# Performance work log

Hardware: AMD Instinct MI355X
Metric: run time of the kernel (lower is better)

## Reference

```python
import jax, jax.numpy as jnp
import numpy as np

N, E, D_IN, H = 40000, 640000, 128, 128
R, B = 8, 30  # num_relations = 2*n_speakers**2, num_bases


def setup_inputs() -> dict:
    key = jax.random.key(0)
    ks = jax.random.split(key, 10)
    node_features = jax.random.normal(ks[0], (N, D_IN), jnp.float32)
    edge_index = jax.random.randint(ks[1], (2, E), 0, N)
    edge_type = jax.random.randint(ks[2], (E,), 0, R)
    edge_norm = jax.random.uniform(ks[3], (E,), jnp.float32)
    s_in = 1.0 / np.sqrt(D_IN)
    s_h = 1.0 / np.sqrt(H)
    basis = jax.random.normal(ks[4], (B, D_IN, H), jnp.float32) * s_in
    comp = jax.random.normal(ks[5], (R, B), jnp.float32) * (1.0 / np.sqrt(B))
    root = jax.random.normal(ks[6], (D_IN, H), jnp.float32) * s_in
    bias1 = jnp.zeros((H,), jnp.float32)
    w_rel = jax.random.normal(ks[7], (H, H), jnp.float32) * s_h
    w_root2 = jax.random.normal(ks[8], (H, H), jnp.float32) * s_h
    bias2 = jnp.zeros((H,), jnp.float32)
    return dict(node_features=node_features, edge_index=edge_index,
                edge_norm=edge_norm, edge_type=edge_type,
                basis=basis, comp=comp, root=root, bias1=bias1,
                w_rel=w_rel, w_root2=w_root2, bias2=bias2)


def reference(node_features, edge_index, edge_norm, edge_type,
              basis, comp, root, bias1, w_rel, w_root2, bias2):
    n = node_features.shape[0]
    src, dst = edge_index[0], edge_index[1]  # messages flow src -> dst

    # ---- RGCNConv (basis decomposition, mean aggregation, root + bias) ----
    # Per-relation weights from bases: [R, D_in, H]
    w = jnp.einsum('rb,bio->rio', comp, basis)
    # Transform all nodes by every relation once (avoids per-edge matmul): [R, N, H]
    xw = jnp.einsum('nd,rdo->rno', node_features, w)
    msgs = xw[edge_type, src]                                  # [E, H]
    agg = jax.ops.segment_sum(msgs, dst, num_segments=n)       # [N, H]
    deg = jax.ops.segment_sum(jnp.ones_like(dst, dtype=node_features.dtype),
                              dst, num_segments=n)
    agg = agg / jnp.maximum(deg, 1.0)[:, None]                 # mean aggregation
    h = agg + node_features @ root + bias1                     # [N, H]

    # ---- GraphConv (add aggregation): W_rel * sum_j x_j + W_root * x_i + b ----
    nbr = jax.ops.segment_sum(h[src], dst, num_segments=n)     # [N, H]
    out = nbr @ w_rel + h @ w_root2 + bias2
    return out
```

## Files before the change

### kernel.cpp

```cpp
#include <hip/hip_runtime.h>
#include <stdint.h>

#define DH 128
#define NB 30
#define NR 8

typedef short bf16x8 __attribute__((ext_vector_type(8)));
typedef float f32x4 __attribute__((ext_vector_type(4)));

static __device__ __forceinline__ unsigned short f2bf(float f) {
    unsigned u = __float_as_uint(f);
    u += 0x7fffu + ((u >> 16) & 1u);
    return (unsigned short)(u >> 16);
}

__global__ __launch_bounds__(256) void k_cvtx(const float* __restrict__ x,
                                              unsigned short* __restrict__ xbf, int n4) {
    int i = blockIdx.x * blockDim.x + threadIdx.x;
    if (i < n4) {
        float4 v = ((const float4*)x)[i];
        ushort4 u;
        u.x = f2bf(v.x); u.y = f2bf(v.y); u.z = f2bf(v.z); u.w = f2bf(v.w);
        ((ushort4*)xbf)[i] = u;
    }
}

__global__ __launch_bounds__(128) void k_wprep(const float* __restrict__ comp,
                                               const float* __restrict__ basis,
                                               const float* __restrict__ root,
                                               const float* __restrict__ wrel,
                                               const float* __restrict__ wroot2,
                                               unsigned short* __restrict__ wallT,
                                               unsigned short* __restrict__ WT2) {
    int o = threadIdx.x;
    int i = blockIdx.x;
    int y = blockIdx.y;
    if (y < NR) {
        float s = 0.f;
        #pragma unroll
        for (int b = 0; b < NB; ++b)
            s += comp[y * NB + b] * basis[((size_t)b * DH + i) * DH + o];
        wallT[((size_t)y * DH + o) * DH + i] = f2bf(s);
    } else if (y == NR) {
        wallT[((size_t)NR * DH + o) * DH + i] = f2bf(root[i * DH + o]);
    } else {
        const float* W = (y == NR + 2) ? wroot2 : wrel;
        WT2[((size_t)(y - NR - 1) * DH + o) * DH + i] = f2bf(W[i * DH + o]);
    }
}

__global__ void k_hist(const int* __restrict__ dst, int E, int* __restrict__ deg) {
    int e = blockIdx.x * blockDim.x + threadIdx.x;
    if (e < E) atomicAdd(&deg[dst[e]], 1);
}

__global__ __launch_bounds__(1024) void k_scan1(const int* __restrict__ deg, int n, int total_n,
                                                int* __restrict__ offsets, int* __restrict__ partial) {
    __shared__ int s[1024];
    int tid = threadIdx.x;
    int i = blockIdx.x * 1024 + tid;
    int v = (i < n) ? deg[i] : 0;
    s[tid] = v;
    __syncthreads();
    for (int off = 1; off < 1024; off <<= 1) {
        int t = (tid >= off) ? s[tid - off] : 0;
        __syncthreads();
        s[tid] += t;
        __syncthreads();
    }
    if (i < total_n) offsets[i] = s[tid] - v;
    if (tid == 1023) partial[blockIdx.x] = s[1023];
}

__global__ void k_scan2(int* __restrict__ partial, int nb) {
    if (threadIdx.x == 0) {
        int run = 0;
        for (int b = 0; b < nb; ++b) { int t = partial[b]; partial[b] = run; run += t; }
    }
}

__global__ __launch_bounds__(1024) void k_scan3(int* __restrict__ offsets,
                                                const int* __restrict__ partial, int total_n) {
    int i = blockIdx.x * 1024 + threadIdx.x;
    if (i < total_n) offsets[i] += partial[blockIdx.x];
}

__global__ void k_scatter(const int* __restrict__ src, const int* __restrict__ dstA,
                          const int* __restrict__ etype, int E,
                          const int* __restrict__ offsets, int* __restrict__ cursor,
                          unsigned* __restrict__ sorted) {
    int e = blockIdx.x * blockDim.x + threadIdx.x;
    if (e >= E) return;
    int d = dstA[e];
    int pos = offsets[d] + atomicAdd(&cursor[d], 1);
    sorted[pos] = (unsigned)src[e] | ((unsigned)etype[e] << 17);
}

__global__ __launch_bounds__(256) void k_gemm1m(const unsigned short* __restrict__ Xbf,
                                                const unsigned short* __restrict__ wallT,
                                                const float* __restrict__ bias1,
                                                int Nn,
                                                unsigned short* __restrict__ xw,
                                                unsigned short* __restrict__ hb) {
    __shared__ __align__(16) unsigned short As[128][136];
    __shared__ __align__(16) unsigned short Bs[128][136];
    const int tid = threadIdx.x;
    const int wave = tid >> 6, lane = tid & 63;
    const int r = blockIdx.y;
    const int rowbase = blockIdx.x * 128;
    const unsigned short* WT = wallT + (size_t)r * DH * DH;

    #pragma unroll
    for (int it = 0; it < 8; ++it) {
        int c = it * 256 + tid;
        int row = c >> 4, col = c & 15;
        int rg = rowbase + row; if (rg >= Nn) rg = Nn - 1;
        *(uint4*)&As[row][col * 8] = *(const uint4*)&Xbf[(size_t)rg * DH + col * 8];
        *(uint4*)&Bs[row][col * 8] = *(const uint4*)&WT[(size_t)row * DH + col * 8];
    }
    __syncthreads();

    f32x4 acc[2][8];
    #pragma unroll
    for (int mt = 0; mt < 2; ++mt)
        #pragma unroll
        for (int nt = 0; nt < 8; ++nt) acc[mt][nt] = (f32x4)0.f;

    const int lq = lane >> 4, lr = lane & 15;
    #pragma unroll
    for (int ks = 0; ks < 4; ++ks) {
        const int ko = ks * 32 + lq * 8;
        bf16x8 a0 = *(const bf16x8*)&As[wave * 32 + lr][ko];
        bf16x8 a1 = *(const bf16x8*)&As[wave * 32 + 16 + lr][ko];
        #pragma unroll
        for (int nt = 0; nt < 8; ++nt) {
            bf16x8 b = *(const bf16x8*)&Bs[nt * 16 + lr][ko];
            acc[0][nt] = __builtin_amdgcn_mfma_f32_16x16x32_bf16(a0, b, acc[0][nt], 0, 0, 0);
            acc[1][nt] = __builtin_amdgcn_mfma_f32_16x16x32_bf16(a1, b, acc[1][nt], 0, 0, 0);
        }
    }

    float bv[8];
    #pragma unroll
    for (int nt = 0; nt < 8; ++nt) bv[nt] = (r == NR) ? bias1[nt * 16 + lr] : 0.f;
    #pragma unroll
    for (int mt = 0; mt < 2; ++mt)
        #pragma unroll
        for (int nt = 0; nt < 8; ++nt)
            #pragma unroll
            for (int reg = 0; reg < 4; ++reg) {
                int ml = wave * 32 + mt * 16 + lq * 4 + reg;
                As[ml][nt * 16 + lr] = f2bf(acc[mt][nt][reg] + bv[nt]);
            }
    __syncthreads();
    unsigned short* dst = (r < NR) ? xw + ((size_t)r * Nn + rowbase) * DH
                                   : hb + (size_t)rowbase * DH;
    #pragma unroll
    for (int it = 0; it < 8; ++it) {
        int c = it * 256 + tid;
        int row = c >> 4, col = c & 15;
        if (rowbase + row < Nn)
            *(uint4*)&dst[(size_t)row * DH + col * 8] = *(uint4*)&As[row][col * 8];
    }
}

__global__ __launch_bounds__(256) void k_agg1(const int* __restrict__ offsets,
                                              const unsigned* __restrict__ sorted,
                                              const unsigned* __restrict__ xw32,
                                              const unsigned* __restrict__ hb32,
                                              int Nn, unsigned* __restrict__ hbf) {
    int w = (blockIdx.x * blockDim.x + threadIdx.x) >> 6;
    if (w >= Nn) return;
    int lane = threadIdx.x & 63;
    int s = offsets[w], e = offsets[w + 1];
    float ax = 0.f, ay = 0.f;
    for (int p = s; p < e; p += 16) {
        unsigned pk[16]; float m[16];
        #pragma unroll
        for (int j = 0; j < 16; ++j) {
            int q = p + j; bool v = q < e;
            pk[j] = sorted[v ? q : e - 1];
            m[j] = v ? 1.f : 0.f;
        }
        unsigned u[16];
        #pragma unroll
        for (int j = 0; j < 16; ++j)
            u[j] = xw32[((size_t)(pk[j] >> 17) * Nn + (pk[j] & 0x1FFFFu)) * 64 + lane];
        #pragma unroll
        for (int j = 0; j < 16; ++j) {
            ax = fmaf(m[j], __uint_as_float(u[j] << 16), ax);
            ay = fmaf(m[j], __uint_as_float(u[j] & 0xffff0000u), ay);
        }
    }
    float invd = 1.0f / fmaxf((float)(e - s), 1.0f);
    unsigned hv = hb32[(size_t)w * 64 + lane];
    float hx = __uint_as_float(hv << 16) + ax * invd;
    float hy = __uint_as_float(hv & 0xffff0000u) + ay * invd;
    hbf[(size_t)w * 64 + lane] = (unsigned)f2bf(hx) | ((unsigned)f2bf(hy) << 16);
}

__global__ __launch_bounds__(256) void k_agg2(const int* __restrict__ offsets,
                                              const unsigned* __restrict__ sorted,
                                              const unsigned* __restrict__ hbf32,
                                              int Nn, unsigned* __restrict__ nbrbf) {
    int w = (blockIdx.x * blockDim.x + threadIdx.x) >> 6;
    if (w >= Nn) return;
    int lane = threadIdx.x & 63;
    int s = offsets[w], e = offsets[w + 1];
    float ax = 0.f, ay = 0.f;
    for (int p = s; p < e; p += 16) {
        unsigned pk[16]; float m[16];
        #pragma unroll
        for (int j = 0; j < 16; ++j) {
            int q = p + j; bool v = q < e;
            pk[j] = sorted[v ? q : e - 1];
            m[j] = v ? 1.f : 0.f;
        }
        unsigned u[16];
        #pragma unroll
        for (int j = 0; j < 16; ++j)
            u[j] = hbf32[(size_t)(pk[j] & 0x1FFFFu) * 64 + lane];
        #pragma unroll
        for (int j = 0; j < 16; ++j) {
            ax = fmaf(m[j], __uint_as_float(u[j] << 16), ax);
            ay = fmaf(m[j], __uint_as_float(u[j] & 0xffff0000u), ay);
        }
    }
    nbrbf[(size_t)w * 64 + lane] = (unsigned)f2bf(ax) | ((unsigned)f2bf(ay) << 16);
}

__global__ __launch_bounds__(256) void k_gemm2m(const unsigned short* __restrict__ nbrbf,
                                                const unsigned short* __restrict__ hbf,
                                                const unsigned short* __restrict__ WT2,
                                                const float* __restrict__ bias2,
                                                int Nn, float* __restrict__ out) {
    __shared__ __align__(16) unsigned short As[128][136];
    __shared__ __align__(16) unsigned short Bs[128][136];
    const int tid = threadIdx.x;
    const int wave = tid >> 6, lane = tid & 63;
    const int rowbase = blockIdx.x * 128;
    const int lq = lane >> 4, lr = lane & 15;

    f32x4 acc[2][8];
    #pragma unroll
    for (int mt = 0; mt < 2; ++mt)
        #pragma unroll
        for (int nt = 0; nt < 8; ++nt) acc[mt][nt] = (f32x4)0.f;

    for (int ph = 0; ph < 2; ++ph) {
        const unsigned short* A = ph ? hbf : nbrbf;
        const unsigned short* WT = WT2 + (size_t)ph * DH * DH;
        if (ph) __syncthreads();
        #pragma unroll
        for (int it = 0; it < 8; ++it) {
            int c = it * 256 + tid;
            int row = c >> 4, col = c & 15;
            int rg = rowbase + row; if (rg >= Nn) rg = Nn - 1;
            *(uint4*)&As[row][col * 8] = *(const uint4*)&A[(size_t)rg * DH + col * 8];
            *(uint4*)&Bs[row][col * 8] = *(const uint4*)&WT[(size_t)row * DH + col * 8];
        }
        __syncthreads();
        #pragma unroll
        for (int ks = 0; ks < 4; ++ks) {
            const int ko = ks * 32 + lq * 8;
            bf16x8 a0 = *(const bf16x8*)&As[wave * 32 + lr][ko];
            bf16x8 a1 = *(const bf16x8*)&As[wave * 32 + 16 + lr][ko];
            #pragma unroll
            for (int nt = 0; nt < 8; ++nt) {
                bf16x8 b = *(const bf16x8*)&Bs[nt * 16 + lr][ko];
                acc[0][nt] = __builtin_amdgcn_mfma_f32_16x16x32_bf16(a0, b, acc[0][nt], 0, 0, 0);
                acc[1][nt] = __builtin_amdgcn_mfma_f32_16x16x32_bf16(a1, b, acc[1][nt], 0, 0, 0);
            }
        }
    }

    float bv[8];
    #pragma unroll
    for (int nt = 0; nt < 8; ++nt) bv[nt] = bias2[nt * 16 + lr];
    #pragma unroll
    for (int mt = 0; mt < 2; ++mt)
        #pragma unroll
        for (int nt = 0; nt < 8; ++nt)
            #pragma unroll
            for (int reg = 0; reg < 4; ++reg) {
                int m = rowbase + wave * 32 + mt * 16 + lq * 4 + reg;
                if (m < Nn) out[(size_t)m * DH + nt * 16 + lr] = acc[mt][nt][reg] + bv[nt];
            }
}

extern "C" void kernel_launch(void* const* d_in, const int* in_sizes, int n_in,
                              void* d_out, int out_size, void* d_ws, size_t ws_size,
                              hipStream_t stream) {
    const float* x      = (const float*)d_in[0];
    const int*   eidx   = (const int*)d_in[1];
    const int*   etype  = (const int*)d_in[3];
    const float* basis  = (const float*)d_in[4];
    const float* comp   = (const float*)d_in[5];
    const float* root   = (const float*)d_in[6];
    const float* bias1  = (const float*)d_in[7];
    const float* wrel   = (const float*)d_in[8];
    const float* wroot2 = (const float*)d_in[9];
    const float* bias2  = (const float*)d_in[10];
    float* out = (float*)d_out;

    const int N = in_sizes[0] / DH;
    const int E = in_sizes[3];
    const int* srcA = eidx;
    const int* dstA = eidx + E;

    char* ws = (char*)d_ws;
    size_t off = 0;
    auto alloc = [&](size_t bytes) -> void* {
        void* p = (void*)(ws + off);
        off += (bytes + 255) & ~(size_t)255;
        return p;
    };
    int* deg           = (int*)alloc((size_t)N * 4);
    int* cursor        = (int*)alloc((size_t)N * 4);
    int* offsets       = (int*)alloc((size_t)(N + 1) * 4);
    int* partial       = (int*)alloc(256 * 4);
    unsigned* sorted   = (unsigned*)alloc((size_t)E * 4);
    unsigned short* wallT = (unsigned short*)alloc((size_t)(NR + 1) * DH * DH * 2);
    unsigned short* WT2   = (unsigned short*)alloc((size_t)2 * DH * DH * 2);
    unsigned short* Xbf   = (unsigned short*)alloc((size_t)N * DH * 2);
    unsigned short* xw    = (unsigned short*)alloc((size_t)NR * N * DH * 2);
    unsigned short* hb    = (unsigned short*)alloc((size_t)N * DH * 2);
    unsigned* hbf      = (unsigned*)alloc((size_t)N * (DH / 2) * 4);
    unsigned* nbrbf    = (unsigned*)alloc((size_t)N * (DH / 2) * 4);
    (void)ws_size; (void)n_in; (void)out_size;

    hipMemsetAsync(deg, 0, (size_t)N * 8, stream);

    k_cvtx<<<(N * DH / 4 + 255) / 256, 256, 0, stream>>>(x, Xbf, N * DH / 4);
    k_wprep<<<dim3(DH, NR + 3), DH, 0, stream>>>(comp, basis, root, wrel, wroot2, wallT, WT2);
    k_hist<<<(E + 255) / 256, 256, 0, stream>>>(dstA, E, deg);

    const int totn = N + 1;
    const int nsb = (totn + 1023) / 1024;
    k_scan1<<<nsb, 1024, 0, stream>>>(deg, N, totn, offsets, partial);
    k_scan2<<<1, 64, 0, stream>>>(partial, nsb);
    k_scan3<<<nsb, 1024, 0, stream>>>(offsets, partial, totn);
    k_scatter<<<(E + 255) / 256, 256, 0, stream>>>(srcA, dstA, etype, E, offsets, cursor, sorted);

    const int gx = (N + 127) / 128;
    k_gemm1m<<<dim3(gx, NR + 1), 256, 0, stream>>>(Xbf, wallT, bias1, N, xw, hb);
    k_agg1<<<(N * 64) / 256, 256, 0, stream>>>(offsets, sorted, (const unsigned*)xw,
                                               (const unsigned*)hb, N, hbf);
    k_agg2<<<(N * 64) / 256, 256, 0, stream>>>(offsets, sorted, hbf, N, nbrbf);
    k_gemm2m<<<gx, 256, 0, stream>>>((const unsigned short*)nbrbf, (const unsigned short*)hbf,
                                     WT2, bias2, N, out);
}
```

Baseline: 267.0 us.

## Store per-relation transformed features as FP8 and gather two edges per wave

The first GEMM now writes per-relation transformed node features as packed FP8 instead of bf16, halving the bytes in the largest intermediate buffer and in the random gathers of the first aggregation. Each GEMM block also reuses its loaded X tile across three relation weight matrices (grid y reduced to 3). The aggregation kernel splits each wave into two halves that handle alternating edges with 4 features per lane, then combines them with a cross-half shuffle. FP8 quantization of messages reduces numerical precision and may risk tolerance failures.

```diff
diff --git a/kernel.cpp b/kernel.cpp
--- a/kernel.cpp
+++ b/kernel.cpp
@@ -7,12 +7,15 @@
 
 typedef short bf16x8 __attribute__((ext_vector_type(8)));
 typedef float f32x4 __attribute__((ext_vector_type(4)));
+typedef float f32x2 __attribute__((ext_vector_type(2)));
 
 static __device__ __forceinline__ unsigned short f2bf(float f) {
     unsigned u = __float_as_uint(f);
     u += 0x7fffu + ((u >> 16) & 1u);
     return (unsigned short)(u >> 16);
 }
+static __device__ __forceinline__ float bflo(unsigned u) { return __uint_as_float(u << 16); }
+static __device__ __forceinline__ float bfhi(unsigned u) { return __uint_as_float(u & 0xffff0000u); }
 
 __global__ __launch_bounds__(256) void k_cvtx(const float* __restrict__ x,
                                               unsigned short* __restrict__ xbf, int n4) {
@@ -100,15 +103,15 @@
                                                 const unsigned short* __restrict__ wallT,
                                                 const float* __restrict__ bias1,
                                                 int Nn,
-                                                unsigned short* __restrict__ xw,
+                                                unsigned* __restrict__ xw8,
                                                 unsigned short* __restrict__ hb) {
     __shared__ __align__(16) unsigned short As[128][136];
     __shared__ __align__(16) unsigned short Bs[128][136];
     const int tid = threadIdx.x;
     const int wave = tid >> 6, lane = tid & 63;
-    const int r = blockIdx.y;
+    const int g = blockIdx.y;
     const int rowbase = blockIdx.x * 128;
-    const unsigned short* WT = wallT + (size_t)r * DH * DH;
+    const int lq = lane >> 4, lr = lane & 15;
 
     #pragma unroll
     for (int it = 0; it < 8; ++it) {
@@ -116,87 +119,131 @@
         int row = c >> 4, col = c & 15;
         int rg = rowbase + row; if (rg >= Nn) rg = Nn - 1;
         *(uint4*)&As[row][col * 8] = *(const uint4*)&Xbf[(size_t)rg * DH + col * 8];
-        *(uint4*)&Bs[row][col * 8] = *(const uint4*)&WT[(size_t)row * DH + col * 8];
-    }
-    __syncthreads();
-
-    f32x4 acc[2][8];
-    #pragma unroll
-    for (int mt = 0; mt < 2; ++mt)
-        #pragma unroll
-        for (int nt = 0; nt < 8; ++nt) acc[mt][nt] = (f32x4)0.f;
-
-    const int lq = lane >> 4, lr = lane & 15;
-    #pragma unroll
-    for (int ks = 0; ks < 4; ++ks) {
-        const int ko = ks * 32 + lq * 8;
-        bf16x8 a0 = *(const bf16x8*)&As[wave * 32 + lr][ko];
-        bf16x8 a1 = *(const bf16x8*)&As[wave * 32 + 16 + lr][ko];
-        #pragma unroll
-        for (int nt = 0; nt < 8; ++nt) {
-            bf16x8 b = *(const bf16x8*)&Bs[nt * 16 + lr][ko];
-            acc[0][nt] = __builtin_amdgcn_mfma_f32_16x16x32_bf16(a0, b, acc[0][nt], 0, 0, 0);
-            acc[1][nt] = __builtin_amdgcn_mfma_f32_16x16x32_bf16(a1, b, acc[1][nt], 0, 0, 0);
-        }
-    }
-
-    float bv[8];
-    #pragma unroll
-    for (int nt = 0; nt < 8; ++nt) bv[nt] = (r == NR) ? bias1[nt * 16 + lr] : 0.f;
-    #pragma unroll
-    for (int mt = 0; mt < 2; ++mt)
-        #pragma unroll
-        for (int nt = 0; nt < 8; ++nt)
-            #pragma unroll
-            for (int reg = 0; reg < 4; ++reg) {
-                int ml = wave * 32 + mt * 16 + lq * 4 + reg;
-                As[ml][nt * 16 + lr] = f2bf(acc[mt][nt][reg] + bv[nt]);
-            }
-    __syncthreads();
-    unsigned short* dst = (r < NR) ? xw + ((size_t)r * Nn + rowbase) * DH
-                                   : hb + (size_t)rowbase * DH;
-    #pragma unroll
-    for (int it = 0; it < 8; ++it) {
-        int c = it * 256 + tid;
-        int row = c >> 4, col = c & 15;
-        if (rowbase + row < Nn)
-            *(uint4*)&dst[(size_t)row * DH + col * 8] = *(uint4*)&As[row][col * 8];
+    }
+
+    for (int rr = 0; rr < 3; ++rr) {
+        const int r = g * 3 + rr;
+        const unsigned short* WT = wallT + (size_t)r * DH * DH;
+        if (rr) __syncthreads();
+        #pragma unroll
+        for (int it = 0; it < 8; ++it) {
+            int c = it * 256 + tid;
+            int row = c >> 4, col = c & 15;
+            *(uint4*)&Bs[row][col * 8] = *(const uint4*)&WT[(size_t)row * DH + col * 8];
+        }
+        __syncthreads();
+
+        f32x4 acc[2][8];
+        #pragma unroll
+        for (int mt = 0; mt < 2; ++mt)
+            #pragma unroll
+            for (int nt = 0; nt < 8; ++nt) acc[mt][nt] = (f32x4)0.f;
+
+        #pragma unroll
+        for (int ks = 0; ks < 4; ++ks) {
+            const int ko = ks * 32 + lq * 8;
+            bf16x8 a0 = *(const bf16x8*)&As[wave * 32 + lr][ko];
+            bf16x8 a1 = *(const bf16x8*)&As[wave * 32 + 16 + lr][ko];
+            #pragma unroll
+            for (int nt = 0; nt < 8; ++nt) {
+                bf16x8 b = *(const bf16x8*)&Bs[nt * 16 + lr][ko];
+                acc[0][nt] = __builtin_amdgcn_mfma_f32_16x16x32_bf16(a0, b, acc[0][nt], 0, 0, 0);
+                acc[1][nt] = __builtin_amdgcn_mfma_f32_16x16x32_bf16(a1, b, acc[1][nt], 0, 0, 0);
+            }
+        }
+        __syncthreads();
+
+        float bv[8];
+        #pragma unroll
+        for (int nt = 0; nt < 8; ++nt) bv[nt] = (r == NR) ? bias1[nt * 16 + lr] : 0.f;
+        #pragma unroll
+        for (int mt = 0; mt < 2; ++mt)
+            #pragma unroll
+            for (int nt = 0; nt < 8; ++nt)
+                #pragma unroll
+                for (int reg = 0; reg < 4; ++reg) {
+                    int ml = wave * 32 + mt * 16 + lq * 4 + reg;
+                    Bs[ml][nt * 16 + lr] = f2bf(acc[mt][nt][reg] + bv[nt]);
+                }
+        __syncthreads();
+
+        if (r < NR) {
+            unsigned* dst = xw8 + ((size_t)r * Nn + rowbase) * (DH / 4);
+            #pragma unroll
+            for (int it = 0; it < 8; ++it) {
+                int c = it * 256 + tid;
+                int row = c >> 4, col = c & 15;
+                if (rowbase + row < Nn) {
+                    uint4 q = *(uint4*)&Bs[row][col * 8];
+                    uint2 o;
+                    o.x = __builtin_amdgcn_cvt_pk_fp8_f32(bflo(q.x), bfhi(q.x), 0, false);
+                    o.x = __builtin_amdgcn_cvt_pk_fp8_f32(bflo(q.y), bfhi(q.y), o.x, true);
+                    o.y = __builtin_amdgcn_cvt_pk_fp8_f32(bflo(q.z), bfhi(q.z), 0, false);
+                    o.y = __builtin_amdgcn_cvt_pk_fp8_f32(bflo(q.w), bfhi(q.w), o.y, true);
+                    *(uint2*)&dst[(size_t)row * (DH / 4) + col * 2] = o;
+                }
+            }
+        } else {
+            #pragma unroll
+            for (int it = 0; it < 8; ++it) {
+                int c = it * 256 + tid;
+                int row = c >> 4, col = c & 15;
+                if (rowbase + row < Nn)
+                    *(uint4*)&hb[((size_t)(rowbase + row)) * DH + col * 8] = *(uint4*)&Bs[row][col * 8];
+            }
+        }
     }
 }
 
 __global__ __launch_bounds__(256) void k_agg1(const int* __restrict__ offsets,
                                               const unsigned* __restrict__ sorted,
-                                              const unsigned* __restrict__ xw32,
+                                              const unsigned* __restrict__ xw8,
                                               const unsigned* __restrict__ hb32,
                                               int Nn, unsigned* __restrict__ hbf) {
     int w = (blockIdx.x * blockDim.x + threadIdx.x) >> 6;
     if (w >= Nn) return;
     int lane = threadIdx.x & 63;
+    int half = lane >> 5, sub = lane & 31;
     int s = offsets[w], e = offsets[w + 1];
-    float ax = 0.f, ay = 0.f;
+    float a0 = 0.f, a1 = 0.f, a2 = 0.f, a3 = 0.f;
     for (int p = s; p < e; p += 16) {
-        unsigned pk[16]; float m[16];
-        #pragma unroll
-        for (int j = 0; j < 16; ++j) {
-            int q = p + j; bool v = q < e;
+        unsigned pk[8]; float m[8];
+        #pragma unroll
+        for (int j = 0; j < 8; ++j) {
+            int q = p + 2 * j + half; bool v = q < e;
             pk[j] = sorted[v ? q : e - 1];
             m[j] = v ? 1.f : 0.f;
         }
-        unsigned u[16];
-        #pragma unroll
-        for (int j = 0; j < 16; ++j)
-            u[j] = xw32[((size_t)(pk[j] >> 17) * Nn + (pk[j] & 0x1FFFFu)) * 64 + lane];
-        #pragma unroll
-        for (int j = 0; j < 16; ++j) {
-            ax = fmaf(m[j], __uint_as_float(u[j] << 16), ax);
-            ay = fmaf(m[j], __uint_as_float(u[j] & 0xffff0000u), ay);
-        }
-    }
-    float invd = 1.0f / fmaxf((float)(e - s), 1.0f);
-    unsigned hv = hb32[(size_t)w * 64 + lane];
-    float hx = __uint_as_float(hv << 16) + ax * invd;
-    float hy = __uint_as_float(hv & 0xffff0000u) + ay * invd;
-    hbf[(size_t)w * 64 + lane] = (unsigned)f2bf(hx) | ((unsigned)f2bf(hy) << 16);
+        unsigned u[8];
+        #pragma unroll
+        for (int j = 0; j < 8; ++j)
+            u[j] = xw8[((size_t)(pk[j] >> 17) * Nn + (pk[j] & 0x1FFFFu)) * 32 + sub];
+        #pragma unroll
+        for (int j = 0; j < 8; ++j) {
+            f32x2 lo = __builtin_amdgcn_cvt_pk_f32_fp8(u[j], false);
+            f32x2 hi = __builtin_amdgcn_cvt_pk_f32_fp8(u[j], true);
+            a0 = fmaf(m[j], lo.x, a0);
+            a1 = fmaf(m[j], lo.y, a1);
+            a2 = fmaf(m[j], hi.x, a2);
+            a3 = fmaf(m[j], hi.y, a3);
+        }
+    }
+    a0 += __shfl_xor(a0, 32, 64);
+    a1 += __shfl_xor(a1, 32, 64);
+    a2 += __shfl_xor(a2, 32, 64);
+    a3 += __shfl_xor(a3, 32, 64);
+    if (half == 0) {
+        float invd = 1.0f / fmaxf((float)(e - s), 1.0f);
+        uint2 hv = *(const uint2*)&hb32[(size_t)w * 64 + sub * 2];
+        float h0 = bflo(hv.x) + a0 * invd;
+        float h1 = bfhi(hv.x) + a1 * invd;
+        float h2 = bflo(hv.y) + a2 * invd;
+        float h3 = bfhi(hv.y) + a3 * invd;
+        uint2 o;
+        o.x = (unsigned)f2bf(h0) | ((unsigned)f2bf(h1) << 16);
+        o.y = (unsigned)f2bf(h2) | ((unsigned)f2bf(h3) << 16);
+        *(uint2*)&hbf[(size_t)w * 64 + sub * 2] = o;
+    }
 }
 
 __global__ __launch_bounds__(256) void k_agg2(const int* __restrict__ offsets,
@@ -323,8 +370,8 @@
     unsigned short* wallT = (unsigned short*)alloc((size_t)(NR + 1) * DH * DH * 2);
     unsigned short* WT2   = (unsigned short*)alloc((size_t)2 * DH * DH * 2);
     unsigned short* Xbf   = (unsigned short*)alloc((size_t)N * DH * 2);
-    unsigned short* xw    = (unsigned short*)alloc((size_t)NR * N * DH * 2);
-    unsigned short* hb    = (unsigned short*)alloc((size_t)N * DH * 2);
+    unsigned* xw8      = (unsigned*)alloc((size_t)NR * N * DH);
+    unsigned short* hb = (unsigned short*)alloc((size_t)N * DH * 2);
     unsigned* hbf      = (unsigned*)alloc((size_t)N * (DH / 2) * 4);
     unsigned* nbrbf    = (unsigned*)alloc((size_t)N * (DH / 2) * 4);
     (void)ws_size; (void)n_in; (void)out_size;
@@ -343,8 +390,8 @@
     k_scatter<<<(E + 255) / 256, 256, 0, stream>>>(srcA, dstA, etype, E, offsets, cursor, sorted);
 
     const int gx = (N + 127) / 128;
-    k_gemm1m<<<dim3(gx, NR + 1), 256, 0, stream>>>(Xbf, wallT, bias1, N, xw, hb);
-    k_agg1<<<(N * 64) / 256, 256, 0, stream>>>(offsets, sorted, (const unsigned*)xw,
+    k_gemm1m<<<dim3(gx, 3), 256, 0, stream>>>(Xbf, wallT, bias1, N, xw8, hb);
+    k_agg1<<<(N * 64) / 256, 256, 0, stream>>>(offsets, sorted, xw8,
                                                (const unsigned*)hb, N, hbf);
     k_agg2<<<(N * 64) / 256, 256, 0, stream>>>(offsets, sorted, hbf, N, nbrbf);
     k_gemm2m<<<gx, 256, 0, stream>>>((const unsigned short*)nbrbf, (const unsigned short*)hbf,
```

New measurement: 252.4 us. 1.06x faster.
